# Kernel optimization log

Hardware: AMD Instinct MI355X
Metric: run time of the kernel (lower is better)

Reference implementation:

```python
import jax, jax.numpy as jnp
import numpy as np

D_MODEL = 1024
NUM_HEADS = 16
D_K = D_MODEL // NUM_HEADS
SCALE = 1.0 / np.sqrt(D_K).astype(np.float32)
NEG_INF = -1.0e9


def setup_inputs() -> dict:
    key = jax.random.key(0)
    ks = jax.random.split(key, 9)
    B, S = 4, 2048
    query = jax.random.normal(ks[0], (B, S, D_MODEL), dtype=jnp.float32)
    key_t = jax.random.normal(ks[1], (B, S, D_MODEL), dtype=jnp.float32)
    value = jax.random.normal(ks[2], (B, S, D_MODEL), dtype=jnp.float32)
    mask = jax.random.randint(ks[3], (B, S), 0, 2, dtype=jnp.int32)
    init = 1.0 / np.sqrt(D_MODEL).astype(np.float32)
    W_q = jax.random.uniform(ks[4], (D_MODEL, D_MODEL), jnp.float32, -init, init)
    W_k = jax.random.uniform(ks[5], (D_MODEL, D_MODEL), jnp.float32, -init, init)
    W_v = jax.random.uniform(ks[6], (D_MODEL, D_MODEL), jnp.float32, -init, init)
    W_o = jax.random.uniform(ks[7], (D_MODEL, D_MODEL), jnp.float32, -init, init)
    b_o = jax.random.uniform(ks[8], (D_MODEL,), jnp.float32, -init, init)
    return {"query": query, "key": key_t, "value": value, "mask": mask,
            "W_q": W_q, "W_k": W_k, "W_v": W_v, "W_o": W_o, "b_o": b_o}


def reference(query, key, value, mask, W_q, W_k, W_v, W_o, b_o):
    B, S, _ = query.shape
    # projections -> [B, H, S, d_k]  (torch Linear: x @ W.T)
    def split_heads(x, W):
        y = jnp.einsum('bsd,ed->bse', x, W)
        return y.reshape(B, S, NUM_HEADS, D_K).transpose(0, 2, 1, 3)
    Q = split_heads(query, W_q)
    K = split_heads(key, W_k)
    V = split_heads(value, W_v)
    # scores [B, H, S, S]
    scores = jnp.einsum('bhqd,bhkd->bhqk', Q, K) * SCALE
    key_mask = (mask[:, None, None, :] != 0)  # [B,1,1,S] over key axis
    scores = jnp.where(key_mask, scores, NEG_INF)
    probs = jax.nn.softmax(scores, axis=-1)
    # dropout is identity (p=0 / eval mode)
    context = jnp.einsum('bhqk,bhkd->bhqd', probs, V)
    context = context.transpose(0, 2, 1, 3).reshape(B, S, D_MODEL)
    output = jnp.einsum('bsd,ed->bse', context, W_o) + b_o
    return output, probs.mean(axis=1)
```

## Files before the change

### kernel.cpp

```cpp
#include <hip/hip_runtime.h>

typedef unsigned short u16t;
typedef __bf16 bf16x8 __attribute__((ext_vector_type(8)));
typedef float f32x4 __attribute__((ext_vector_type(4)));

#define NB 4
#define NS 2048
#define ND 1024
#define NH 16
#define NDK 64
#define SCALE_ 0.125f
#define NEGINF -1.0e9f

#define LKV 72
#define LAB 40

__device__ __forceinline__ bf16x8 load8_cvt(const float* p) {
  const f32x4 a = *(const f32x4*)p;
  const f32x4 b = *(const f32x4*)(p + 4);
  bf16x8 r;
  r[0] = (__bf16)a[0]; r[1] = (__bf16)a[1]; r[2] = (__bf16)a[2]; r[3] = (__bf16)a[3];
  r[4] = (__bf16)b[0]; r[5] = (__bf16)b[1]; r[6] = (__bf16)b[2]; r[7] = (__bf16)b[3];
  return r;
}
__device__ __forceinline__ bf16x8 load8_cvt(const u16t* p) {
  return *(const bf16x8*)p;
}
__device__ __forceinline__ u16t f2bf(float f) {
  unsigned u = __builtin_bit_cast(unsigned, f);
  u += 0x7fffu + ((u >> 16) & 1u);
  return (u16t)(u >> 16);
}

template<typename TA, int MODE>
__global__ __launch_bounds__(256, 2)
void gemm_nt(const TA* __restrict__ A, const float* __restrict__ Bm,
             void* __restrict__ Cv, const float* __restrict__ bias)
{
  const int K = 1024;
  __shared__ __attribute__((aligned(16))) u16t At[128 * LAB];
  __shared__ __attribute__((aligned(16))) u16t Bt[128 * LAB];

  const int tid  = threadIdx.x;
  const int w    = tid >> 6;
  const int lane = tid & 63;
  const int quad = lane >> 4;
  const int l16  = lane & 15;
  const int wm   = w >> 1, wn = w & 1;
  const int m0   = blockIdx.x * 128;
  const int n0   = blockIdx.y * 128;

  const f32x4 fz = {0.f, 0.f, 0.f, 0.f};
  f32x4 acc[4][4];
#pragma unroll
  for (int i = 0; i < 4; i++)
#pragma unroll
    for (int j = 0; j < 4; j++) acc[i][j] = fz;

  const int r0 = tid >> 2, cg = (tid & 3) * 8;
  const int r1 = r0 + 64;

  for (int k0 = 0; k0 < K; k0 += 32) {
    bf16x8 va0 = load8_cvt(A  + (long)(m0 + r0) * K + k0 + cg);
    bf16x8 va1 = load8_cvt(A  + (long)(m0 + r1) * K + k0 + cg);
    bf16x8 vb0 = load8_cvt(Bm + (long)(n0 + r0) * K + k0 + cg);
    bf16x8 vb1 = load8_cvt(Bm + (long)(n0 + r1) * K + k0 + cg);
    __syncthreads();
    *(bf16x8*)&At[r0 * LAB + cg] = va0;
    *(bf16x8*)&At[r1 * LAB + cg] = va1;
    *(bf16x8*)&Bt[r0 * LAB + cg] = vb0;
    *(bf16x8*)&Bt[r1 * LAB + cg] = vb1;
    __syncthreads();

    bf16x8 af[4], bfv[4];
#pragma unroll
    for (int i = 0; i < 4; i++)
      af[i] = *(const bf16x8*)&At[(wm * 64 + i * 16 + l16) * LAB + quad * 8];
#pragma unroll
    for (int j = 0; j < 4; j++)
      bfv[j] = *(const bf16x8*)&Bt[(wn * 64 + j * 16 + l16) * LAB + quad * 8];
#pragma unroll
    for (int i = 0; i < 4; i++)
#pragma unroll
      for (int j = 0; j < 4; j++)
        acc[i][j] = __builtin_amdgcn_mfma_f32_16x16x32_bf16(af[i], bfv[j], acc[i][j], 0, 0, 0);
  }

#pragma unroll
  for (int i = 0; i < 4; i++) {
    const int rbase = m0 + wm * 64 + i * 16 + quad * 4;
#pragma unroll
    for (int j = 0; j < 4; j++) {
      const int col = n0 + wn * 64 + j * 16 + l16;
      float bv = 0.f;
      if (MODE == 0) bv = bias[col];
#pragma unroll
      for (int r = 0; r < 4; r++) {
        const int row = rbase + r;
        float v = acc[i][j][r];
        if (MODE == 0) {
          ((float*)Cv)[(long)row * ND + col] = v + bv;
        } else if (MODE == 1) {
          int b = row >> 11, s = row & 2047, h = col >> 6, d = col & 63;
          ((u16t*)Cv)[(((long)(b * NH + h)) * NS + s) * NDK + d] = f2bf(v);
        } else {
          int b = row >> 11, s = row & 2047, h = col >> 6, d = col & 63;
          ((u16t*)Cv)[(((long)(b * NH + h)) * NDK + d) * NS + s] = f2bf(v);
        }
      }
    }
  }
}

__global__ __launch_bounds__(256, 3)
void flash_ctx(const u16t* __restrict__ Qw, const u16t* __restrict__ Kw,
               const u16t* __restrict__ VTw, const int* __restrict__ mask,
               u16t* __restrict__ ctx, float* __restrict__ mo, float* __restrict__ lo)
{
  __shared__ __attribute__((aligned(16))) u16t Kt[64 * LKV];
  __shared__ __attribute__((aligned(16))) u16t Vt[64 * LKV];
  __shared__ __attribute__((aligned(16))) u16t Pt[4 * 32 * LKV];
  __shared__ float biasl[NS];

  const int tid  = threadIdx.x;
  const int w    = tid >> 6;
  const int lane = tid & 63;
  const int quad = lane >> 4;
  const int l16  = lane & 15;
  const int bh   = blockIdx.y;
  const int b    = bh >> 4;
  const int h    = bh & 15;
  const int qw   = blockIdx.x * 128 + w * 32;

  for (int i = tid; i < NS; i += 256)
    biasl[i] = mask[b * NS + i] ? 0.f : NEGINF;

  bf16x8 qf[2][2];
#pragma unroll
  for (int g = 0; g < 2; g++)
#pragma unroll
    for (int kk = 0; kk < 2; kk++)
      qf[g][kk] = *(const bf16x8*)(Qw + ((long)bh * NS + qw + g * 16 + l16) * NDK + kk * 32 + quad * 8);

  const f32x4 fz = {0.f, 0.f, 0.f, 0.f};
  const f32x4 fm = {NEGINF, NEGINF, NEGINF, NEGINF};
  f32x4 cacc[2][4];
#pragma unroll
  for (int g = 0; g < 2; g++)
#pragma unroll
    for (int d = 0; d < 4; d++) cacc[g][d] = fz;
  f32x4 mrun[2] = {fm, fm};
  f32x4 lrun[2] = {fz, fz};

  const int kr0 = tid >> 3, kc0 = (tid & 7) * 8;
  const int kr1 = kr0 + 32;

  for (int kb = 0; kb < NS; kb += 64) {
    bf16x8 k0v = *(const bf16x8*)(Kw  + ((long)bh * NS + kb + kr0) * NDK + kc0);
    bf16x8 k1v = *(const bf16x8*)(Kw  + ((long)bh * NS + kb + kr1) * NDK + kc0);
    bf16x8 v0v = *(const bf16x8*)(VTw + ((long)bh * NDK + kr0) * NS + kb + kc0);
    bf16x8 v1v = *(const bf16x8*)(VTw + ((long)bh * NDK + kr1) * NS + kb + kc0);
    __syncthreads();
    *(bf16x8*)&Kt[kr0 * LKV + kc0] = k0v;
    *(bf16x8*)&Kt[kr1 * LKV + kc0] = k1v;
    *(bf16x8*)&Vt[kr0 * LKV + kc0] = v0v;
    *(bf16x8*)&Vt[kr1 * LKV + kc0] = v1v;
    __syncthreads();

    f32x4 s[2][4];
#pragma unroll
    for (int g = 0; g < 2; g++)
#pragma unroll
      for (int c = 0; c < 4; c++) {
        f32x4 a = fz;
#pragma unroll
        for (int kk = 0; kk < 2; kk++) {
          bf16x8 kf = *(const bf16x8*)&Kt[(c * 16 + l16) * LKV + kk * 32 + quad * 8];
          a = __builtin_amdgcn_mfma_f32_16x16x32_bf16(qf[g][kk], kf, a, 0, 0, 0);
        }
        s[g][c] = a;
      }

    float bias_c[4];
#pragma unroll
    for (int c = 0; c < 4; c++) bias_c[c] = biasl[kb + c * 16 + l16];

#pragma unroll
    for (int g = 0; g < 2; g++) {
#pragma unroll
      for (int c = 0; c < 4; c++)
#pragma unroll
        for (int r = 0; r < 4; r++)
          s[g][c][r] = s[g][c][r] * SCALE_ + bias_c[c];

      f32x4 mx = s[g][0];
#pragma unroll
      for (int c = 1; c < 4; c++)
#pragma unroll
        for (int r = 0; r < 4; r++) mx[r] = fmaxf(mx[r], s[g][c][r]);
#pragma unroll
      for (int off = 1; off < 16; off <<= 1)
#pragma unroll
        for (int r = 0; r < 4; r++) mx[r] = fmaxf(mx[r], __shfl_xor(mx[r], off, 64));

      f32x4 alpha;
#pragma unroll
      for (int r = 0; r < 4; r++) {
        float mnew = fmaxf(mrun[g][r], mx[r]);
        alpha[r] = __expf(mrun[g][r] - mnew);
        mrun[g][r] = mnew;
      }
#pragma unroll
      for (int c = 0; c < 4; c++)
#pragma unroll
        for (int r = 0; r < 4; r++) s[g][c][r] = __expf(s[g][c][r] - mrun[g][r]);

      f32x4 sm = fz;
#pragma unroll
      for (int c = 0; c < 4; c++)
#pragma unroll
        for (int r = 0; r < 4; r++) sm[r] += s[g][c][r];
#pragma unroll
      for (int off = 1; off < 16; off <<= 1)
#pragma unroll
        for (int r = 0; r < 4; r++) sm[r] += __shfl_xor(sm[r], off, 64);
#pragma unroll
      for (int r = 0; r < 4; r++) lrun[g][r] = lrun[g][r] * alpha[r] + sm[r];
#pragma unroll
      for (int d = 0; d < 4; d++)
#pragma unroll
        for (int r = 0; r < 4; r++) cacc[g][d][r] *= alpha[r];

#pragma unroll
      for (int c = 0; c < 4; c++)
#pragma unroll
        for (int r = 0; r < 4; r++)
          Pt[w * 32 * LKV + (g * 16 + quad * 4 + r) * LKV + c * 16 + l16] = f2bf(s[g][c][r]);
    }

#pragma unroll
    for (int g = 0; g < 2; g++)
#pragma unroll
      for (int d = 0; d < 4; d++)
#pragma unroll
        for (int kk = 0; kk < 2; kk++) {
          bf16x8 pf = *(const bf16x8*)&Pt[w * 32 * LKV + (g * 16 + l16) * LKV + kk * 32 + quad * 8];
          bf16x8 vf = *(const bf16x8*)&Vt[(d * 16 + l16) * LKV + kk * 32 + quad * 8];
          cacc[g][d] = __builtin_amdgcn_mfma_f32_16x16x32_bf16(pf, vf, cacc[g][d], 0, 0, 0);
        }
  }

#pragma unroll
  for (int g = 0; g < 2; g++) {
    f32x4 rinv;
#pragma unroll
    for (int r = 0; r < 4; r++) rinv[r] = 1.f / lrun[g][r];
#pragma unroll
    for (int d = 0; d < 4; d++)
#pragma unroll
      for (int r = 0; r < 4; r++) {
        int qg = qw + g * 16 + quad * 4 + r;
        int e  = h * NDK + d * 16 + l16;
        ctx[((long)(b * NS + qg)) * ND + e] = f2bf(cacc[g][d][r] * rinv[r]);
      }
    if (l16 == 0) {
#pragma unroll
      for (int r = 0; r < 4; r++) {
        int qg = qw + g * 16 + quad * 4 + r;
        mo[(long)bh * NS + qg] = mrun[g][r];
        lo[(long)bh * NS + qg] = lrun[g][r];
      }
    }
  }
}

__global__ __launch_bounds__(256, 2)
void probs_mean(const u16t* __restrict__ Qw, const u16t* __restrict__ Kw,
                const int* __restrict__ mask, const float* __restrict__ mo,
                const float* __restrict__ lo, float* __restrict__ outp)
{
  __shared__ __attribute__((aligned(16))) u16t Qt[128 * LKV];
  __shared__ __attribute__((aligned(16))) u16t Kt2[128 * LKV];
  __shared__ float ml[NH * 128];
  __shared__ float li[NH * 128];
  __shared__ float biasl[128];

  const int tid  = threadIdx.x;
  const int w    = tid >> 6;
  const int lane = tid & 63;
  const int quad = lane >> 4;
  const int l16  = lane & 15;
  const int wm   = w >> 1, wn = w & 1;
  const int b  = blockIdx.z;
  const int q0 = blockIdx.y * 128;
  const int k0 = blockIdx.x * 128;

  for (int i = tid; i < NH * 128; i += 256) {
    int hh = i >> 7, r = i & 127;
    ml[i] = mo[((long)(b * NH + hh)) * NS + q0 + r];
    li[i] = 1.f / lo[((long)(b * NH + hh)) * NS + q0 + r];
  }
  for (int i = tid; i < 128; i += 256)
    biasl[i] = mask[b * NS + k0 + i] ? 0.f : NEGINF;

  const f32x4 fz = {0.f, 0.f, 0.f, 0.f};
  f32x4 acc[4][4];
#pragma unroll
  for (int i = 0; i < 4; i++)
#pragma unroll
    for (int j = 0; j < 4; j++) acc[i][j] = fz;

  for (int hh = 0; hh < NH; hh++) {
    bf16x8 qv[4], kv[4];
#pragma unroll
    for (int rr = 0; rr < 4; rr++) {
      int idx = rr * 256 + tid;
      int row = idx >> 3, off = (idx & 7) * 8;
      qv[rr] = *(const bf16x8*)(Qw + ((long)(b * NH + hh) * NS + q0 + row) * NDK + off);
      kv[rr] = *(const bf16x8*)(Kw + ((long)(b * NH + hh) * NS + k0 + row) * NDK + off);
    }
    __syncthreads();
#pragma unroll
    for (int rr = 0; rr < 4; rr++) {
      int idx = rr * 256 + tid;
      int row = idx >> 3, off = (idx & 7) * 8;
      *(bf16x8*)&Qt[row * LKV + off]  = qv[rr];
      *(bf16x8*)&Kt2[row * LKV + off] = kv[rr];
    }
    __syncthreads();

    bf16x8 af[4][2], bfv[4][2];
#pragma unroll
    for (int i = 0; i < 4; i++)
#pragma unroll
      for (int kk = 0; kk < 2; kk++) {
        af[i][kk]  = *(const bf16x8*)&Qt[(wm * 64 + i * 16 + l16) * LKV + kk * 32 + quad * 8];
        bfv[i][kk] = *(const bf16x8*)&Kt2[(wn * 64 + i * 16 + l16) * LKV + kk * 32 + quad * 8];
      }
#pragma unroll
    for (int i = 0; i < 4; i++)
#pragma unroll
      for (int j = 0; j < 4; j++) {
        f32x4 s = fz;
#pragma unroll
        for (int kk = 0; kk < 2; kk++)
          s = __builtin_amdgcn_mfma_f32_16x16x32_bf16(af[i][kk], bfv[j][kk], s, 0, 0, 0);
        const float bias_c = biasl[wn * 64 + j * 16 + l16];
#pragma unroll
        for (int r = 0; r < 4; r++) {
          int rowb = wm * 64 + i * 16 + quad * 4 + r;
          float p = __expf(s[r] * SCALE_ + bias_c - ml[hh * 128 + rowb]) * li[hh * 128 + rowb];
          acc[i][j][r] += p;
        }
      }
  }

#pragma unroll
  for (int i = 0; i < 4; i++)
#pragma unroll
    for (int j = 0; j < 4; j++)
#pragma unroll
      for (int r = 0; r < 4; r++) {
        int row = q0 + wm * 64 + i * 16 + quad * 4 + r;
        int col = k0 + wn * 64 + j * 16 + l16;
        outp[((long)(b * NS + row)) * NS + col] = acc[i][j][r] * (1.f / 16.f);
      }
}

extern "C" void kernel_launch(void* const* d_in, const int* in_sizes, int n_in,
                              void* d_out, int out_size, void* d_ws, size_t ws_size,
                              hipStream_t stream)
{
  (void)in_sizes; (void)n_in; (void)out_size; (void)ws_size;
  const float* query = (const float*)d_in[0];
  const float* keyt  = (const float*)d_in[1];
  const float* value = (const float*)d_in[2];
  const int*   mask  = (const int*)d_in[3];
  const float* Wq = (const float*)d_in[4];
  const float* Wk = (const float*)d_in[5];
  const float* Wv = (const float*)d_in[6];
  const float* Wo = (const float*)d_in[7];
  const float* bo = (const float*)d_in[8];

  float* out  = (float*)d_out;
  float* outp = out + (long)NB * NS * ND;

  u16t* q_ws  = (u16t*)d_ws;
  u16t* k_ws  = q_ws + (long)NB * NH * NS * NDK;
  u16t* vt_ws = k_ws + (long)NB * NH * NS * NDK;
  float* m_ws = (float*)(vt_ws + (long)NB * NH * NS * NDK);
  float* l_ws = m_ws + (long)NB * NH * NS;
  u16t* ctx_ws = (u16t*)outp;

  dim3 blk(256);
  gemm_nt<float, 1><<<dim3(64, 8), blk, 0, stream>>>(query, Wq, q_ws, nullptr);
  gemm_nt<float, 1><<<dim3(64, 8), blk, 0, stream>>>(keyt,  Wk, k_ws, nullptr);
  gemm_nt<float, 2><<<dim3(64, 8), blk, 0, stream>>>(value, Wv, vt_ws, nullptr);
  flash_ctx<<<dim3(NS / 128, NB * NH), blk, 0, stream>>>(q_ws, k_ws, vt_ws, mask,
                                                         ctx_ws, m_ws, l_ws);
  gemm_nt<u16t, 0><<<dim3(64, 8), blk, 0, stream>>>(ctx_ws, Wo, out, bo);
  probs_mean<<<dim3(NS / 128, NS / 128, NB), blk, 0, stream>>>(q_ws, k_ws, mask,
                                                               m_ws, l_ws, outp);
}
```

Before: 615.9 us.

## Prefetch global tiles, swizzle LDS, use exp2 and DPP reductions in attention

Register-prefetches the next K-tile in the projection GEMM, flash kernel and probs kernel so global loads overlap MFMA work. Replaces padded LDS rows in the flash kernel with an XOR swizzle, and raises its occupancy hint from 3 to 4 blocks. Switches softmax to base-2 exponentials with a log2e-folded scale and uses DPP row-rotate reductions instead of shuffles. Rescaling of the running accumulators is skipped unless some row's max grows. Prefetch registers may raise register pressure against the tighter launch bound.

```diff
diff --git a/kernel.cpp b/kernel.cpp
--- a/kernel.cpp
+++ b/kernel.cpp
@@ -9,28 +9,46 @@
 #define ND 1024
 #define NH 16
 #define NDK 64
-#define SCALE_ 0.125f
 #define NEGINF -1.0e9f
-
+#define SCALE2 0.18033688011112042f
+
+#define LAB 40
 #define LKV 72
-#define LAB 40
-
-__device__ __forceinline__ bf16x8 load8_cvt(const float* p) {
-  const f32x4 a = *(const f32x4*)p;
-  const f32x4 b = *(const f32x4*)(p + 4);
-  bf16x8 r;
-  r[0] = (__bf16)a[0]; r[1] = (__bf16)a[1]; r[2] = (__bf16)a[2]; r[3] = (__bf16)a[3];
-  r[4] = (__bf16)b[0]; r[5] = (__bf16)b[1]; r[6] = (__bf16)b[2]; r[7] = (__bf16)b[3];
-  return r;
-}
-__device__ __forceinline__ bf16x8 load8_cvt(const u16t* p) {
-  return *(const bf16x8*)p;
-}
+
+__device__ __forceinline__ float fexp2(float x) { return __builtin_amdgcn_exp2f(x); }
+
+#define ROR16(x, n) __builtin_bit_cast(float, __builtin_amdgcn_update_dpp(     \
+    __builtin_bit_cast(int, (x)), __builtin_bit_cast(int, (x)),                \
+    0x120 + (n), 0xF, 0xF, false))
+
 __device__ __forceinline__ u16t f2bf(float f) {
   unsigned u = __builtin_bit_cast(unsigned, f);
   u += 0x7fffu + ((u >> 16) & 1u);
   return (u16t)(u >> 16);
 }
+
+__device__ __forceinline__ int swz(int row, int col) {
+  return row * 64 + (col ^ ((row & 7) << 3));
+}
+
+template<typename TA> struct Stg;
+template<> struct Stg<float> {
+  f32x4 lo, hi;
+  __device__ __forceinline__ void ld(const float* p) {
+    lo = *(const f32x4*)p; hi = *(const f32x4*)(p + 4);
+  }
+  __device__ __forceinline__ bf16x8 get() const {
+    bf16x8 r;
+    r[0] = (__bf16)lo[0]; r[1] = (__bf16)lo[1]; r[2] = (__bf16)lo[2]; r[3] = (__bf16)lo[3];
+    r[4] = (__bf16)hi[0]; r[5] = (__bf16)hi[1]; r[6] = (__bf16)hi[2]; r[7] = (__bf16)hi[3];
+    return r;
+  }
+};
+template<> struct Stg<u16t> {
+  bf16x8 v;
+  __device__ __forceinline__ void ld(const u16t* p) { v = *(const bf16x8*)p; }
+  __device__ __forceinline__ bf16x8 get() const { return v; }
+};
 
 template<typename TA, int MODE>
 __global__ __launch_bounds__(256, 2)
@@ -60,17 +78,25 @@
   const int r0 = tid >> 2, cg = (tid & 3) * 8;
   const int r1 = r0 + 64;
 
+  Stg<TA> sa0, sa1; Stg<float> sb0, sb1;
+  sa0.ld(A  + (long)(m0 + r0) * K + cg);
+  sa1.ld(A  + (long)(m0 + r1) * K + cg);
+  sb0.ld(Bm + (long)(n0 + r0) * K + cg);
+  sb1.ld(Bm + (long)(n0 + r1) * K + cg);
+
   for (int k0 = 0; k0 < K; k0 += 32) {
-    bf16x8 va0 = load8_cvt(A  + (long)(m0 + r0) * K + k0 + cg);
-    bf16x8 va1 = load8_cvt(A  + (long)(m0 + r1) * K + k0 + cg);
-    bf16x8 vb0 = load8_cvt(Bm + (long)(n0 + r0) * K + k0 + cg);
-    bf16x8 vb1 = load8_cvt(Bm + (long)(n0 + r1) * K + k0 + cg);
-    __syncthreads();
-    *(bf16x8*)&At[r0 * LAB + cg] = va0;
-    *(bf16x8*)&At[r1 * LAB + cg] = va1;
-    *(bf16x8*)&Bt[r0 * LAB + cg] = vb0;
-    *(bf16x8*)&Bt[r1 * LAB + cg] = vb1;
-    __syncthreads();
+    __syncthreads();
+    *(bf16x8*)&At[r0 * LAB + cg] = sa0.get();
+    *(bf16x8*)&At[r1 * LAB + cg] = sa1.get();
+    *(bf16x8*)&Bt[r0 * LAB + cg] = sb0.get();
+    *(bf16x8*)&Bt[r1 * LAB + cg] = sb1.get();
+    __syncthreads();
+    if (k0 + 32 < K) {
+      sa0.ld(A  + (long)(m0 + r0) * K + k0 + 32 + cg);
+      sa1.ld(A  + (long)(m0 + r1) * K + k0 + 32 + cg);
+      sb0.ld(Bm + (long)(n0 + r0) * K + k0 + 32 + cg);
+      sb1.ld(Bm + (long)(n0 + r1) * K + k0 + 32 + cg);
+    }
 
     bf16x8 af[4], bfv[4];
 #pragma unroll
@@ -112,14 +138,14 @@
   }
 }
 
-__global__ __launch_bounds__(256, 3)
+__global__ __launch_bounds__(256, 4)
 void flash_ctx(const u16t* __restrict__ Qw, const u16t* __restrict__ Kw,
                const u16t* __restrict__ VTw, const int* __restrict__ mask,
                u16t* __restrict__ ctx, float* __restrict__ mo, float* __restrict__ lo)
 {
-  __shared__ __attribute__((aligned(16))) u16t Kt[64 * LKV];
-  __shared__ __attribute__((aligned(16))) u16t Vt[64 * LKV];
-  __shared__ __attribute__((aligned(16))) u16t Pt[4 * 32 * LKV];
+  __shared__ __attribute__((aligned(16))) u16t Kt[64 * 64];
+  __shared__ __attribute__((aligned(16))) u16t Vt[64 * 64];
+  __shared__ __attribute__((aligned(16))) u16t Pt[4 * 32 * 64];
   __shared__ float biasl[NS];
 
   const int tid  = threadIdx.x;
@@ -131,6 +157,7 @@
   const int b    = bh >> 4;
   const int h    = bh & 15;
   const int qw   = blockIdx.x * 128 + w * 32;
+  const int pbase = w * 2048;
 
   for (int i = tid; i < NS; i += 256)
     biasl[i] = mask[b * NS + i] ? 0.f : NEGINF;
@@ -154,18 +181,27 @@
 
   const int kr0 = tid >> 3, kc0 = (tid & 7) * 8;
   const int kr1 = kr0 + 32;
+  const long kbase = (long)bh * NS;
+  const long vbase = (long)bh * NDK;
+
+  bf16x8 k0v = *(const bf16x8*)(Kw  + (kbase + kr0) * NDK + kc0);
+  bf16x8 k1v = *(const bf16x8*)(Kw  + (kbase + kr1) * NDK + kc0);
+  bf16x8 v0v = *(const bf16x8*)(VTw + (vbase + kr0) * NS + kc0);
+  bf16x8 v1v = *(const bf16x8*)(VTw + (vbase + kr1) * NS + kc0);
 
   for (int kb = 0; kb < NS; kb += 64) {
-    bf16x8 k0v = *(const bf16x8*)(Kw  + ((long)bh * NS + kb + kr0) * NDK + kc0);
-    bf16x8 k1v = *(const bf16x8*)(Kw  + ((long)bh * NS + kb + kr1) * NDK + kc0);
-    bf16x8 v0v = *(const bf16x8*)(VTw + ((long)bh * NDK + kr0) * NS + kb + kc0);
-    bf16x8 v1v = *(const bf16x8*)(VTw + ((long)bh * NDK + kr1) * NS + kb + kc0);
-    __syncthreads();
-    *(bf16x8*)&Kt[kr0 * LKV + kc0] = k0v;
-    *(bf16x8*)&Kt[kr1 * LKV + kc0] = k1v;
-    *(bf16x8*)&Vt[kr0 * LKV + kc0] = v0v;
-    *(bf16x8*)&Vt[kr1 * LKV + kc0] = v1v;
-    __syncthreads();
+    __syncthreads();
+    *(bf16x8*)&Kt[swz(kr0, kc0)] = k0v;
+    *(bf16x8*)&Kt[swz(kr1, kc0)] = k1v;
+    *(bf16x8*)&Vt[swz(kr0, kc0)] = v0v;
+    *(bf16x8*)&Vt[swz(kr1, kc0)] = v1v;
+    __syncthreads();
+    if (kb + 64 < NS) {
+      k0v = *(const bf16x8*)(Kw  + (kbase + kb + 64 + kr0) * NDK + kc0);
+      k1v = *(const bf16x8*)(Kw  + (kbase + kb + 64 + kr1) * NDK + kc0);
+      v0v = *(const bf16x8*)(VTw + (vbase + kr0) * NS + kb + 64 + kc0);
+      v1v = *(const bf16x8*)(VTw + (vbase + kr1) * NS + kb + 64 + kc0);
+    }
 
     f32x4 s[2][4];
 #pragma unroll
@@ -175,7 +211,7 @@
         f32x4 a = fz;
 #pragma unroll
         for (int kk = 0; kk < 2; kk++) {
-          bf16x8 kf = *(const bf16x8*)&Kt[(c * 16 + l16) * LKV + kk * 32 + quad * 8];
+          bf16x8 kf = *(const bf16x8*)&Kt[swz(c * 16 + l16, kk * 32 + quad * 8)];
           a = __builtin_amdgcn_mfma_f32_16x16x32_bf16(qf[g][kk], kf, a, 0, 0, 0);
         }
         s[g][c] = a;
@@ -191,7 +227,7 @@
       for (int c = 0; c < 4; c++)
 #pragma unroll
         for (int r = 0; r < 4; r++)
-          s[g][c][r] = s[g][c][r] * SCALE_ + bias_c[c];
+          s[g][c][r] = s[g][c][r] * SCALE2 + bias_c[c];
 
       f32x4 mx = s[g][0];
 #pragma unroll
@@ -199,21 +235,33 @@
 #pragma unroll
         for (int r = 0; r < 4; r++) mx[r] = fmaxf(mx[r], s[g][c][r]);
 #pragma unroll
-      for (int off = 1; off < 16; off <<= 1)
-#pragma unroll
-        for (int r = 0; r < 4; r++) mx[r] = fmaxf(mx[r], __shfl_xor(mx[r], off, 64));
-
-      f32x4 alpha;
-#pragma unroll
-      for (int r = 0; r < 4; r++) {
-        float mnew = fmaxf(mrun[g][r], mx[r]);
-        alpha[r] = __expf(mrun[g][r] - mnew);
-        mrun[g][r] = mnew;
-      }
+      for (int r = 0; r < 4; r++) {
+        float x = mx[r];
+        x = fmaxf(x, ROR16(x, 1));
+        x = fmaxf(x, ROR16(x, 2));
+        x = fmaxf(x, ROR16(x, 4));
+        x = fmaxf(x, ROR16(x, 8));
+        mx[r] = x;
+      }
+
+      bool grow = (mx[0] > mrun[g][0]) | (mx[1] > mrun[g][1]) |
+                  (mx[2] > mrun[g][2]) | (mx[3] > mrun[g][3]);
+      if (__any((int)grow)) {
+#pragma unroll
+        for (int r = 0; r < 4; r++) {
+          float mnew = fmaxf(mrun[g][r], mx[r]);
+          float al = fexp2(mrun[g][r] - mnew);
+          mrun[g][r] = mnew;
+          lrun[g][r] *= al;
+#pragma unroll
+          for (int d = 0; d < 4; d++) cacc[g][d][r] *= al;
+        }
+      }
+
 #pragma unroll
       for (int c = 0; c < 4; c++)
 #pragma unroll
-        for (int r = 0; r < 4; r++) s[g][c][r] = __expf(s[g][c][r] - mrun[g][r]);
+        for (int r = 0; r < 4; r++) s[g][c][r] = fexp2(s[g][c][r] - mrun[g][r]);
 
       f32x4 sm = fz;
 #pragma unroll
@@ -221,31 +269,30 @@
 #pragma unroll
         for (int r = 0; r < 4; r++) sm[r] += s[g][c][r];
 #pragma unroll
-      for (int off = 1; off < 16; off <<= 1)
-#pragma unroll
-        for (int r = 0; r < 4; r++) sm[r] += __shfl_xor(sm[r], off, 64);
-#pragma unroll
-      for (int r = 0; r < 4; r++) lrun[g][r] = lrun[g][r] * alpha[r] + sm[r];
+      for (int r = 0; r < 4; r++) {
+        float x = sm[r];
+        x += ROR16(x, 1);
+        x += ROR16(x, 2);
+        x += ROR16(x, 4);
+        x += ROR16(x, 8);
+        lrun[g][r] += x;
+      }
+
+#pragma unroll
+      for (int c = 0; c < 4; c++)
+#pragma unroll
+        for (int r = 0; r < 4; r++)
+          Pt[pbase + swz(g * 16 + quad * 4 + r, c * 16 + l16)] = f2bf(s[g][c][r]);
+    }
+
+#pragma unroll
+    for (int g = 0; g < 2; g++)
 #pragma unroll
       for (int d = 0; d < 4; d++)
 #pragma unroll
-        for (int r = 0; r < 4; r++) cacc[g][d][r] *= alpha[r];
-
-#pragma unroll
-      for (int c = 0; c < 4; c++)
-#pragma unroll
-        for (int r = 0; r < 4; r++)
-          Pt[w * 32 * LKV + (g * 16 + quad * 4 + r) * LKV + c * 16 + l16] = f2bf(s[g][c][r]);
-    }
-
-#pragma unroll
-    for (int g = 0; g < 2; g++)
-#pragma unroll
-      for (int d = 0; d < 4; d++)
-#pragma unroll
         for (int kk = 0; kk < 2; kk++) {
-          bf16x8 pf = *(const bf16x8*)&Pt[w * 32 * LKV + (g * 16 + l16) * LKV + kk * 32 + quad * 8];
-          bf16x8 vf = *(const bf16x8*)&Vt[(d * 16 + l16) * LKV + kk * 32 + quad * 8];
+          bf16x8 pf = *(const bf16x8*)&Pt[pbase + swz(g * 16 + l16, kk * 32 + quad * 8)];
+          bf16x8 vf = *(const bf16x8*)&Vt[swz(d * 16 + l16, kk * 32 + quad * 8)];
           cacc[g][d] = __builtin_amdgcn_mfma_f32_16x16x32_bf16(pf, vf, cacc[g][d], 0, 0, 0);
         }
   }
@@ -310,15 +357,16 @@
 #pragma unroll
     for (int j = 0; j < 4; j++) acc[i][j] = fz;
 
+  bf16x8 qv[4], kv[4];
+#pragma unroll
+  for (int rr = 0; rr < 4; rr++) {
+    int idx = rr * 256 + tid;
+    int row = idx >> 3, off = (idx & 7) * 8;
+    qv[rr] = *(const bf16x8*)(Qw + ((long)(b * NH) * NS + q0 + row) * NDK + off);
+    kv[rr] = *(const bf16x8*)(Kw + ((long)(b * NH) * NS + k0 + row) * NDK + off);
+  }
+
   for (int hh = 0; hh < NH; hh++) {
-    bf16x8 qv[4], kv[4];
-#pragma unroll
-    for (int rr = 0; rr < 4; rr++) {
-      int idx = rr * 256 + tid;
-      int row = idx >> 3, off = (idx & 7) * 8;
-      qv[rr] = *(const bf16x8*)(Qw + ((long)(b * NH + hh) * NS + q0 + row) * NDK + off);
-      kv[rr] = *(const bf16x8*)(Kw + ((long)(b * NH + hh) * NS + k0 + row) * NDK + off);
-    }
     __syncthreads();
 #pragma unroll
     for (int rr = 0; rr < 4; rr++) {
@@ -328,6 +376,15 @@
       *(bf16x8*)&Kt2[row * LKV + off] = kv[rr];
     }
     __syncthreads();
+    if (hh + 1 < NH) {
+#pragma unroll
+      for (int rr = 0; rr < 4; rr++) {
+        int idx = rr * 256 + tid;
+        int row = idx >> 3, off = (idx & 7) * 8;
+        qv[rr] = *(const bf16x8*)(Qw + ((long)(b * NH + hh + 1) * NS + q0 + row) * NDK + off);
+        kv[rr] = *(const bf16x8*)(Kw + ((long)(b * NH + hh + 1) * NS + k0 + row) * NDK + off);
+      }
+    }
 
     bf16x8 af[4][2], bfv[4][2];
 #pragma unroll
@@ -349,7 +406,7 @@
 #pragma unroll
         for (int r = 0; r < 4; r++) {
           int rowb = wm * 64 + i * 16 + quad * 4 + r;
-          float p = __expf(s[r] * SCALE_ + bias_c - ml[hh * 128 + rowb]) * li[hh * 128 + rowb];
+          float p = fexp2(s[r] * SCALE2 + bias_c - ml[hh * 128 + rowb]) * li[hh * 128 + rowb];
           acc[i][j][r] += p;
         }
       }
```

After: 856.6 us. 39.1% more time.
